# Kernel optimization log

Hardware: AMD Instinct MI355X
Metric: run time of the kernel (lower is better)

The kernel has to match this reference:

```python
import jax, jax.numpy as jnp
import numpy as np

N_HEAD = 16

def _rope_cos_sin(T, head_dim, dtype):
    # inv_freq over even indices, freqs [T, head_dim//2]
    inv_freq = 1.0 / (10000.0 ** (jnp.arange(0, head_dim, 2, dtype=jnp.float32) / head_dim))
    t = jnp.arange(T, dtype=jnp.float32)
    freqs = t[:, None] * inv_freq[None, :]
    cos = jnp.cos(freqs).astype(dtype)[None, :, None, :]  # [1,T,1,hd/2]
    sin = jnp.sin(freqs).astype(dtype)[None, :, None, :]
    return cos, sin

def _apply_rope(x, cos, sin):
    # x: [B,T,H,hd]; interleaved halves as in the torch module
    x1, x2 = x[..., ::2], x[..., 1::2]
    return jnp.concatenate([x1 * cos - x2 * sin, x1 * sin + x2 * cos], axis=-1)

def setup_inputs() -> dict:
    key = jax.random.key(0)
    k1, k2, k3 = jax.random.split(key, 3)
    B, T, C = 2, 2048, 1024
    x = jax.random.normal(k1, (B, T, C), dtype=jnp.float32)
    # causal mask (mask==0 positions get -inf), broadcast over B and heads
    attn_mask = jnp.tril(jnp.ones((T, T), dtype=bool))[None, None, :, :]
    w_qkv = jax.random.normal(k2, (C, 3 * C), dtype=jnp.float32) * (1.0 / np.sqrt(C))
    w_out = jax.random.normal(k3, (C, C), dtype=jnp.float32) * (1.0 / np.sqrt(C))
    return {"x": x, "attn_mask": attn_mask, "w_qkv": w_qkv, "w_out": w_out}

def reference(x, attn_mask, w_qkv, w_out):
    B, T, C = x.shape
    H = N_HEAD
    hd = C // H
    qkv = x @ w_qkv  # [B,T,3C]
    q, k, v = jnp.split(qkv, 3, axis=2)
    q = q.reshape(B, T, H, hd)
    k = k.reshape(B, T, H, hd)
    v = v.reshape(B, T, H, hd)
    cos, sin = _rope_cos_sin(T, hd, x.dtype)
    q = _apply_rope(q, cos, sin)
    k = _apply_rope(k, cos, sin)
    scale = 1.0 / np.sqrt(hd).astype(np.float32)
    att = jnp.einsum('bthd,bshd->bhts', q, k) * scale  # [B,H,T,T]
    att = jnp.where(attn_mask, att, -jnp.inf)
    att = jax.nn.softmax(att, axis=-1)
    out = jnp.einsum('bhts,bshd->bthd', att, v).reshape(B, T, C)
    out = out @ w_out
    k_t = jnp.transpose(k, (0, 2, 1, 3))  # [B,H,T,hd]
    v_t = jnp.transpose(v, (0, 2, 1, 3))
    return out, k_t, v_t
```

## Files before the change

kernel.cpp:

```cpp
#include <hip/hip_runtime.h>

#define T_SEQ 2048
#define NH    16
#define HD    64
#define CDIM  1024
#define BDIM  2

using floatx4 = __attribute__((ext_vector_type(4))) float;
using bf16x8  = __attribute__((ext_vector_type(8))) __bf16;
using half4   = __attribute__((ext_vector_type(4))) _Float16;
typedef unsigned short u16;

__device__ __forceinline__ u16 f2bf(float f) {
  unsigned int u = __float_as_uint(f);
  u += 0x7fffu + ((u >> 16) & 1u);
  return (u16)(u >> 16);
}
__device__ __forceinline__ float bf2f(u16 h) {
  return __uint_as_float(((unsigned int)h) << 16);
}
__device__ __forceinline__ u16 f2h(float f) {
  union { _Float16 h; u16 u; } c; c.h = (_Float16)f; return c.u;
}
__device__ __forceinline__ unsigned pk2h(float a, float b) {
  return __builtin_bit_cast(unsigned, __builtin_amdgcn_cvt_pkrtz(a, b));
}
__device__ __forceinline__ void gld16(const void* g, const void* l) {
  __builtin_amdgcn_global_load_lds(
      (const __attribute__((address_space(1))) unsigned int*)(unsigned long long)g,
      (__attribute__((address_space(3))) unsigned int*)(unsigned int)(unsigned long long)l,
      16, 0, 0);
}

__global__ __launch_bounds__(256) void cast_bf16(const float* __restrict__ in,
                                                 u16* __restrict__ out, int n4) {
  int i = blockIdx.x * 256 + threadIdx.x;
  if (i < n4) {
    float4 v = ((const float4*)in)[i];
    ushort4 o;
    o.x = f2bf(v.x); o.y = f2bf(v.y); o.z = f2bf(v.z); o.w = f2bf(v.w);
    ((ushort4*)out)[i] = o;
  }
}

__global__ __launch_bounds__(256) void transpose_cast(const float* __restrict__ W,
                                                      u16* __restrict__ WT,
                                                      int K, int N) {
  __shared__ float tile[32][33];
  int n0 = blockIdx.x * 32, k0 = blockIdx.y * 32;
  int tx = threadIdx.x, ty = threadIdx.y;
#pragma unroll
  for (int i = 0; i < 32; i += 8)
    tile[ty + i][tx] = W[(size_t)(k0 + ty + i) * N + n0 + tx];
  __syncthreads();
#pragma unroll
  for (int i = 0; i < 32; i += 8)
    WT[(size_t)(n0 + ty + i) * K + k0 + tx] = f2bf(tile[tx][ty + i]);
}

template <bool OUT_F32>
__global__ __launch_bounds__(256) void gemm_bt(const u16* __restrict__ A,
                                               const u16* __restrict__ BT,
                                               float* __restrict__ Cf,
                                               u16* __restrict__ Cb,
                                               int M, int N, int K) {
  __shared__ u16 As[128 * 32];
  __shared__ u16 Bs[128 * 32];
  const int tid  = threadIdx.x;
  const int lane = tid & 63, wave = tid >> 6;
  const int quad = lane >> 4, l16 = lane & 15;
  const int wm = (wave & 1) * 64, wn = (wave >> 1) * 64;
  const int row0 = blockIdx.x * 128, col0 = blockIdx.y * 128;
  const int srow = tid >> 2;
  const int sc   = tid & 3;
  const int sgc  = (sc ^ ((srow >> 1) & 3)) * 8;
  floatx4 acc[4][4] = {};
  for (int k0 = 0; k0 < K; k0 += 32) {
    __syncthreads();
    gld16(A  + (size_t)(row0 + srow     ) * K + k0 + sgc, &As[srow * 32 + sc * 8]);
    gld16(A  + (size_t)(row0 + srow + 64) * K + k0 + sgc, &As[(srow + 64) * 32 + sc * 8]);
    gld16(BT + (size_t)(col0 + srow     ) * K + k0 + sgc, &Bs[srow * 32 + sc * 8]);
    gld16(BT + (size_t)(col0 + srow + 64) * K + k0 + sgc, &Bs[(srow + 64) * 32 + sc * 8]);
    __syncthreads();
    bf16x8 af[4], bfv[4];
#pragma unroll
    for (int mt = 0; mt < 4; mt++) {
      int r = wm + mt * 16 + l16;
      af[mt] = *(const bf16x8*)&As[r * 32 + (quad ^ ((r >> 1) & 3)) * 8];
    }
#pragma unroll
    for (int nt = 0; nt < 4; nt++) {
      int r = wn + nt * 16 + l16;
      bfv[nt] = *(const bf16x8*)&Bs[r * 32 + (quad ^ ((r >> 1) & 3)) * 8];
    }
#pragma unroll
    for (int mt = 0; mt < 4; mt++)
#pragma unroll
      for (int nt = 0; nt < 4; nt++)
        acc[mt][nt] = __builtin_amdgcn_mfma_f32_16x16x32_bf16(af[mt], bfv[nt], acc[mt][nt], 0, 0, 0);
  }
#pragma unroll
  for (int mt = 0; mt < 4; mt++)
#pragma unroll
    for (int nt = 0; nt < 4; nt++)
#pragma unroll
      for (int r = 0; r < 4; r++) {
        int row = row0 + wm + mt * 16 + quad * 4 + r;
        int col = col0 + wn + nt * 16 + l16;
        float v = acc[mt][nt][r];
        if (OUT_F32) Cf[(size_t)row * N + col] = v;
        else         Cb[(size_t)row * N + col] = f2bf(v);
      }
}

__global__ __launch_bounds__(256) void rope_qk(const u16* __restrict__ qkv,
                                               u16* __restrict__ qf16,
                                               u16* __restrict__ kf16,
                                               float* __restrict__ kt_out) {
  int gid = blockIdx.x * 4 + (threadIdx.x >> 6);
  int d   = threadIdx.x & 63;
  int t   = gid & (T_SEQ - 1);
  int h   = (gid >> 11) & 15;
  int b   = gid >> 15;
  const u16* qrow = qkv + ((size_t)(b * T_SEQ + t)) * 3072 + h * 64;
  int i = d & 31;
  unsigned int qp = *(const unsigned int*)(qrow + 2 * i);
  unsigned int kp = *(const unsigned int*)(qrow + 1024 + 2 * i);
  float q1 = bf2f((u16)qp), q2 = bf2f((u16)(qp >> 16));
  float k1 = bf2f((u16)kp), k2 = bf2f((u16)(kp >> 16));
  float inv = expf((float)i * -0.28782313662425572f);
  float ang = (float)t * inv;
  float sn = sinf(ang), cs = cosf(ang);
  float qv = (d < 32) ? (q1 * cs - q2 * sn) : (q1 * sn + q2 * cs);
  float kv = (d < 32) ? (k1 * cs - k2 * sn) : (k1 * sn + k2 * cs);
  size_t o = (size_t)gid * 64 + d;
  qf16[o] = f2h(qv * 0.18033688011112042f);
  kf16[o] = f2h(kv);
  kt_out[o] = kv;
}

__global__ __launch_bounds__(256) void v_pack(const u16* __restrict__ qkv,
                                              float* __restrict__ vt_out,
                                              u16* __restrict__ vtf) {
  __shared__ float tile[64][65];
  int blk = blockIdx.x;
  int t0 = (blk & 31) * 64;
  int bh = blk >> 5;
  int b = bh >> 4, h = bh & 15;
  int tx = threadIdx.x & 63, ty = threadIdx.x >> 6;
#pragma unroll
  for (int i = ty; i < 64; i += 4) {
    float v = bf2f(qkv[((size_t)(b * T_SEQ + t0 + i)) * 3072 + 2048 + h * 64 + tx]);
    tile[i][tx] = v;
    vt_out[((size_t)bh * T_SEQ + t0 + i) * 64 + tx] = v;
  }
  __syncthreads();
#pragma unroll
  for (int i = ty; i < 64; i += 4)
    vtf[((size_t)bh * 64 + i) * T_SEQ + t0 + tx] = f2h(tile[tx][i]);
}

__global__ __launch_bounds__(256) void attn_fused(const u16* __restrict__ qf16,
                                                  const u16* __restrict__ kf16,
                                                  const u16* __restrict__ vtf,
                                                  u16* __restrict__ Ob) {
  __shared__ u16 Ks[128 * 64];
  __shared__ u16 Vts[64 * 128];
  const int tid = threadIdx.x;
  const int lane = tid & 63, wave = tid >> 6;
  const int quad = lane >> 4, l16 = lane & 15;
  const int qh2 = quad >> 1, ql2 = (quad & 1) * 4;
  const int qt2 = 31 - (blockIdx.x >> 5);
  const int bh  = blockIdx.x & 31;
  const int t0  = qt2 * 64;
  const int tw  = t0 + wave * 16;

  const u16* Qg = qf16 + ((size_t)bh * T_SEQ + tw) * HD;
  half4 qfrag[4];
#pragma unroll
  for (int kc = 0; kc < 4; kc++)
    qfrag[kc] = *(const half4*)&Qg[(size_t)l16 * HD + kc * 16 + quad * 4];

  floatx4 oacc[4] = {};
  float mrow = -1e30f, lrow = 0.f;
  const int nkt = (qt2 >> 1) + 1;

  for (int kt = 0; kt < nkt; kt++) {
    __syncthreads();
    const size_t koff = ((size_t)bh * T_SEQ + kt * 128) * HD;
    const u16* Vg = vtf + (size_t)bh * HD * T_SEQ + kt * 128;
#pragma unroll
    for (int j = 0; j < 4; j++) {
      int t2 = j * 256 + tid;
      int r = t2 >> 3, c = t2 & 7;
      gld16(kf16 + koff + r * HD + (c ^ (r & 7)) * 8, &Ks[t2 * 8]);
    }
#pragma unroll
    for (int j = 0; j < 4; j++) {
      int t2 = j * 256 + tid;
      int r = t2 >> 4, c = t2 & 15;
      gld16(Vg + (size_t)r * T_SEQ + (c ^ (r & 15)) * 8, &Vts[t2 * 8]);
    }
    __syncthreads();

    floatx4 sacc[8] = {};
#pragma unroll
    for (int kc = 0; kc < 4; kc++)
#pragma unroll
      for (int st = 0; st < 8; st++) {
        int srow = st * 16 + l16;
        half4 ak = *(const half4*)&Ks[srow * 64 + (((kc * 2 + qh2) ^ (srow & 7)) * 8) + ql2];
        sacc[st] = __builtin_amdgcn_mfma_f32_16x16x16f16(ak, qfrag[kc], sacc[st], 0, 0, 0);
      }
    if (kt == nkt - 1) {
      int tg = tw + l16;
#pragma unroll
      for (int st = 0; st < 8; st++) {
        int sg = kt * 128 + st * 16 + quad * 4;
#pragma unroll
        for (int r = 0; r < 4; r++)
          if (sg + r > tg) sacc[st][r] = -1e30f;
      }
    }
    {
      floatx4 vm = sacc[0];
#pragma unroll
      for (int st = 1; st < 8; st++) {
        vm[0] = fmaxf(vm[0], sacc[st][0]); vm[1] = fmaxf(vm[1], sacc[st][1]);
        vm[2] = fmaxf(vm[2], sacc[st][2]); vm[3] = fmaxf(vm[3], sacc[st][3]);
      }
      float mx = fmaxf(fmaxf(vm[0], vm[1]), fmaxf(vm[2], vm[3]));
      mx = fmaxf(mx, __shfl_xor(mx, 16));
      mx = fmaxf(mx, __shfl_xor(mx, 32));
      float mnew = fmaxf(mrow, mx);
      float alpha = exp2f(mrow - mnew);
      mrow = mnew;
      floatx4 vs = {0.f, 0.f, 0.f, 0.f};
#pragma unroll
      for (int st = 0; st < 8; st++) {
#pragma unroll
        for (int r = 0; r < 4; r++) sacc[st][r] = exp2f(sacc[st][r] - mnew);
        vs += sacc[st];
      }
      float rs = (vs[0] + vs[1]) + (vs[2] + vs[3]);
      rs += __shfl_xor(rs, 16);
      rs += __shfl_xor(rs, 32);
      lrow = lrow * alpha + rs;
#pragma unroll
      for (int dt = 0; dt < 4; dt++) oacc[dt] *= alpha;
    }
#pragma unroll
    for (int st = 0; st < 8; st++) {
      union { unsigned u[2]; half4 h; } pc;
      pc.u[0] = pk2h(sacc[st][0], sacc[st][1]);
      pc.u[1] = pk2h(sacc[st][2], sacc[st][3]);
      half4 bp = pc.h;
#pragma unroll
      for (int dt = 0; dt < 4; dt++) {
        int drow = dt * 16 + l16;
        half4 av = *(const half4*)&Vts[drow * 128 + (((st * 2 + qh2) ^ (drow & 15)) * 8) + ql2];
        oacc[dt] = __builtin_amdgcn_mfma_f32_16x16x16f16(av, bp, oacc[dt], 0, 0, 0);
      }
    }
  }
  const int b = bh >> 4, h = bh & 15;
  {
    int t = tw + l16;
    float invl = 1.f / lrow;
#pragma unroll
    for (int dt = 0; dt < 4; dt++) {
      int d0 = dt * 16 + quad * 4;
      ushort4 o;
      o.x = f2bf(oacc[dt][0] * invl);
      o.y = f2bf(oacc[dt][1] * invl);
      o.z = f2bf(oacc[dt][2] * invl);
      o.w = f2bf(oacc[dt][3] * invl);
      *(ushort4*)&Ob[((size_t)(b * T_SEQ) + t) * CDIM + h * HD + d0] = o;
    }
  }
}

extern "C" void kernel_launch(void* const* d_in, const int* in_sizes, int n_in,
                              void* d_out, int out_size, void* d_ws, size_t ws_size,
                              hipStream_t stream) {
  const float* x     = (const float*)d_in[0];
  const float* w_qkv = (const float*)d_in[2];
  const float* w_out = (const float*)d_in[3];
  float* out    = (float*)d_out;
  float* kt_out = out + (size_t)BDIM * T_SEQ * CDIM;
  float* vt_out = kt_out + (size_t)BDIM * T_SEQ * CDIM;

  const size_t F = (size_t)4194304;
  char* base = (char*)d_ws;
  u16* xb   = (u16*)base;
  u16* wqT  = xb + F;
  u16* woT  = wqT + (size_t)3145728;
  u16* qkvb = woT + (size_t)1048576;
  u16* qf16 = qkvb + (size_t)3 * F;
  u16* kf16 = qf16 + F;
  u16* vtf  = (u16*)base;
  u16* Ob   = kf16 + F;

  cast_bf16<<<4096, 256, 0, stream>>>(x, xb, 1048576);
  transpose_cast<<<dim3(96, 32), dim3(32, 8), 0, stream>>>(w_qkv, wqT, 1024, 3072);
  transpose_cast<<<dim3(32, 32), dim3(32, 8), 0, stream>>>(w_out, woT, 1024, 1024);
  gemm_bt<false><<<dim3(32, 24), 256, 0, stream>>>(xb, wqT, (float*)nullptr, qkvb, 4096, 3072, 1024);
  rope_qk<<<16384, 256, 0, stream>>>(qkvb, qf16, kf16, kt_out);
  v_pack<<<1024, 256, 0, stream>>>(qkvb, vt_out, vtf);
  attn_fused<<<1024, 256, 0, stream>>>(qf16, kf16, vtf, Ob);
  gemm_bt<true><<<dim3(32, 8), 256, 0, stream>>>(Ob, woT, out, (u16*)nullptr, 4096, 1024, 1024);
}
```

Baseline: 234.2 us.

## Merge preprocessing kernels, pair causal tiles per attention block, use 32-wide MFMA

Three preprocessing launches (x cast and two weight transposes) become one kernel, and rope and V packing become one kernel, cutting launch overhead. The attention kernel now handles two query tiles per block (j and 31-j), so each block does the same amount of causal work, and it launches 512 blocks instead of 1024. The QK^T product moves from 16x16x16 f16 MFMA to 16x16x32 f16 with half8 fragments, which halves the instruction count for that step. The cost is fewer attention blocks in flight, which gives less parallelism to hide latency.

After: 224.7 us. -4.1%, faster.

```diff
diff --git a/kernel.cpp b/kernel.cpp
--- a/kernel.cpp
+++ b/kernel.cpp
@@ -9,6 +9,7 @@
 using floatx4 = __attribute__((ext_vector_type(4))) float;
 using bf16x8  = __attribute__((ext_vector_type(8))) __bf16;
 using half4   = __attribute__((ext_vector_type(4))) _Float16;
+using half8   = __attribute__((ext_vector_type(8))) _Float16;
 typedef unsigned short u16;
 
 __device__ __forceinline__ u16 f2bf(float f) {
@@ -32,23 +33,32 @@
       16, 0, 0);
 }
 
-__global__ __launch_bounds__(256) void cast_bf16(const float* __restrict__ in,
-                                                 u16* __restrict__ out, int n4) {
-  int i = blockIdx.x * 256 + threadIdx.x;
-  if (i < n4) {
-    float4 v = ((const float4*)in)[i];
+__global__ __launch_bounds__(256) void preproc(const float* __restrict__ x,
+                                               const float* __restrict__ w_qkv,
+                                               const float* __restrict__ w_out,
+                                               u16* __restrict__ xb,
+                                               u16* __restrict__ wqT,
+                                               u16* __restrict__ woT) {
+  __shared__ float tile[32][33];
+  int blk = blockIdx.x, tid = threadIdx.x;
+  if (blk < 4096) {
+    int i = blk * 256 + tid;
+    float4 v = ((const float4*)x)[i];
     ushort4 o;
     o.x = f2bf(v.x); o.y = f2bf(v.y); o.z = f2bf(v.z); o.w = f2bf(v.w);
-    ((ushort4*)out)[i] = o;
-  }
-}
-
-__global__ __launch_bounds__(256) void transpose_cast(const float* __restrict__ W,
-                                                      u16* __restrict__ WT,
-                                                      int K, int N) {
-  __shared__ float tile[32][33];
-  int n0 = blockIdx.x * 32, k0 = blockIdx.y * 32;
-  int tx = threadIdx.x, ty = threadIdx.y;
+    ((ushort4*)xb)[i] = o;
+    return;
+  }
+  const float* W; u16* WT; int K, N, bx, by;
+  if (blk < 4096 + 3072) {
+    int idx = blk - 4096; W = w_qkv; WT = wqT; K = 1024; N = 3072;
+    bx = idx % 96; by = idx / 96;
+  } else {
+    int idx = blk - 7168; W = w_out; WT = woT; K = 1024; N = 1024;
+    bx = idx & 31; by = idx >> 5;
+  }
+  int n0 = bx * 32, k0 = by * 32;
+  int tx = tid & 31, ty = tid >> 5;
 #pragma unroll
   for (int i = 0; i < 32; i += 8)
     tile[ty + i][tx] = W[(size_t)(k0 + ty + i) * N + n0 + tx];
@@ -113,39 +123,40 @@
       }
 }
 
-__global__ __launch_bounds__(256) void rope_qk(const u16* __restrict__ qkv,
-                                               u16* __restrict__ qf16,
-                                               u16* __restrict__ kf16,
-                                               float* __restrict__ kt_out) {
-  int gid = blockIdx.x * 4 + (threadIdx.x >> 6);
-  int d   = threadIdx.x & 63;
-  int t   = gid & (T_SEQ - 1);
-  int h   = (gid >> 11) & 15;
-  int b   = gid >> 15;
-  const u16* qrow = qkv + ((size_t)(b * T_SEQ + t)) * 3072 + h * 64;
-  int i = d & 31;
-  unsigned int qp = *(const unsigned int*)(qrow + 2 * i);
-  unsigned int kp = *(const unsigned int*)(qrow + 1024 + 2 * i);
-  float q1 = bf2f((u16)qp), q2 = bf2f((u16)(qp >> 16));
-  float k1 = bf2f((u16)kp), k2 = bf2f((u16)(kp >> 16));
-  float inv = expf((float)i * -0.28782313662425572f);
-  float ang = (float)t * inv;
-  float sn = sinf(ang), cs = cosf(ang);
-  float qv = (d < 32) ? (q1 * cs - q2 * sn) : (q1 * sn + q2 * cs);
-  float kv = (d < 32) ? (k1 * cs - k2 * sn) : (k1 * sn + k2 * cs);
-  size_t o = (size_t)gid * 64 + d;
-  qf16[o] = f2h(qv * 0.18033688011112042f);
-  kf16[o] = f2h(kv);
-  kt_out[o] = kv;
-}
-
-__global__ __launch_bounds__(256) void v_pack(const u16* __restrict__ qkv,
-                                              float* __restrict__ vt_out,
-                                              u16* __restrict__ vtf) {
+__global__ __launch_bounds__(256) void rope_vpack(const u16* __restrict__ qkv,
+                                                  u16* __restrict__ qf16,
+                                                  u16* __restrict__ kf16,
+                                                  float* __restrict__ kt_out,
+                                                  float* __restrict__ vt_out,
+                                                  u16* __restrict__ vtf) {
+  int blk = blockIdx.x;
+  if (blk < 16384) {
+    int gid = blk * 4 + (threadIdx.x >> 6);
+    int d   = threadIdx.x & 63;
+    int t   = gid & (T_SEQ - 1);
+    int h   = (gid >> 11) & 15;
+    int b   = gid >> 15;
+    const u16* qrow = qkv + ((size_t)(b * T_SEQ + t)) * 3072 + h * 64;
+    int i = d & 31;
+    unsigned int qp = *(const unsigned int*)(qrow + 2 * i);
+    unsigned int kp = *(const unsigned int*)(qrow + 1024 + 2 * i);
+    float q1 = bf2f((u16)qp), q2 = bf2f((u16)(qp >> 16));
+    float k1 = bf2f((u16)kp), k2 = bf2f((u16)(kp >> 16));
+    float inv = expf((float)i * -0.28782313662425572f);
+    float ang = (float)t * inv;
+    float sn = sinf(ang), cs = cosf(ang);
+    float qv = (d < 32) ? (q1 * cs - q2 * sn) : (q1 * sn + q2 * cs);
+    float kv = (d < 32) ? (k1 * cs - k2 * sn) : (k1 * sn + k2 * cs);
+    size_t o = (size_t)gid * 64 + d;
+    qf16[o] = f2h(qv * 0.18033688011112042f);
+    kf16[o] = f2h(kv);
+    kt_out[o] = kv;
+    return;
+  }
   __shared__ float tile[64][65];
-  int blk = blockIdx.x;
-  int t0 = (blk & 31) * 64;
-  int bh = blk >> 5;
+  int b2 = blk - 16384;
+  int t0 = (b2 & 31) * 64;
+  int bh = b2 >> 5;
   int b = bh >> 4, h = bh & 15;
   int tx = threadIdx.x & 63, ty = threadIdx.x >> 6;
 #pragma unroll
@@ -170,112 +181,115 @@
   const int lane = tid & 63, wave = tid >> 6;
   const int quad = lane >> 4, l16 = lane & 15;
   const int qh2 = quad >> 1, ql2 = (quad & 1) * 4;
-  const int qt2 = 31 - (blockIdx.x >> 5);
+  const int j   = blockIdx.x >> 5;
   const int bh  = blockIdx.x & 31;
-  const int t0  = qt2 * 64;
-  const int tw  = t0 + wave * 16;
-
-  const u16* Qg = qf16 + ((size_t)bh * T_SEQ + tw) * HD;
-  half4 qfrag[4];
-#pragma unroll
-  for (int kc = 0; kc < 4; kc++)
-    qfrag[kc] = *(const half4*)&Qg[(size_t)l16 * HD + kc * 16 + quad * 4];
-
-  floatx4 oacc[4] = {};
-  float mrow = -1e30f, lrow = 0.f;
-  const int nkt = (qt2 >> 1) + 1;
-
-  for (int kt = 0; kt < nkt; kt++) {
-    __syncthreads();
-    const size_t koff = ((size_t)bh * T_SEQ + kt * 128) * HD;
-    const u16* Vg = vtf + (size_t)bh * HD * T_SEQ + kt * 128;
-#pragma unroll
-    for (int j = 0; j < 4; j++) {
-      int t2 = j * 256 + tid;
-      int r = t2 >> 3, c = t2 & 7;
-      gld16(kf16 + koff + r * HD + (c ^ (r & 7)) * 8, &Ks[t2 * 8]);
-    }
-#pragma unroll
-    for (int j = 0; j < 4; j++) {
-      int t2 = j * 256 + tid;
-      int r = t2 >> 4, c = t2 & 15;
-      gld16(Vg + (size_t)r * T_SEQ + (c ^ (r & 15)) * 8, &Vts[t2 * 8]);
-    }
-    __syncthreads();
-
-    floatx4 sacc[8] = {};
-#pragma unroll
-    for (int kc = 0; kc < 4; kc++)
+  const int b = bh >> 4, h = bh & 15;
+
+#pragma unroll 1
+  for (int s2 = 0; s2 < 2; s2++) {
+    const int qt2 = s2 ? j : (31 - j);
+    const int tw  = qt2 * 64 + wave * 16;
+    const u16* Qg = qf16 + ((size_t)bh * T_SEQ + tw) * HD;
+    half8 qfrag[2];
+#pragma unroll
+    for (int kc = 0; kc < 2; kc++)
+      qfrag[kc] = *(const half8*)&Qg[(size_t)l16 * HD + kc * 32 + quad * 8];
+
+    floatx4 oacc[4] = {};
+    float mrow = -1e30f, lrow = 0.f;
+    const int nkt = (qt2 >> 1) + 1;
+
+    for (int kt = 0; kt < nkt; kt++) {
+      __syncthreads();
+      const size_t koff = ((size_t)bh * T_SEQ + kt * 128) * HD;
+      const u16* Vg = vtf + (size_t)bh * HD * T_SEQ + kt * 128;
+#pragma unroll
+      for (int jj = 0; jj < 4; jj++) {
+        int t2 = jj * 256 + tid;
+        int r = t2 >> 3, c = t2 & 7;
+        gld16(kf16 + koff + r * HD + (c ^ (r & 7)) * 8, &Ks[t2 * 8]);
+      }
+#pragma unroll
+      for (int jj = 0; jj < 4; jj++) {
+        int t2 = jj * 256 + tid;
+        int r = t2 >> 4, c = t2 & 15;
+        gld16(Vg + (size_t)r * T_SEQ + (c ^ (r & 15)) * 8, &Vts[t2 * 8]);
+      }
+      __syncthreads();
+
+      floatx4 sacc[8] = {};
+#pragma unroll
+      for (int kc = 0; kc < 2; kc++)
+#pragma unroll
+        for (int st = 0; st < 8; st++) {
+          int srow = st * 16 + l16;
+          half8 ak = *(const half8*)&Ks[srow * 64 + (((kc * 4 + quad) ^ (srow & 7)) * 8)];
+          sacc[st] = __builtin_amdgcn_mfma_f32_16x16x32_f16(ak, qfrag[kc], sacc[st], 0, 0, 0);
+        }
+      if (kt == nkt - 1) {
+        int tg = tw + l16;
+#pragma unroll
+        for (int st = 0; st < 8; st++) {
+          int sg = kt * 128 + st * 16 + quad * 4;
+#pragma unroll
+          for (int r = 0; r < 4; r++)
+            if (sg + r > tg) sacc[st][r] = -1e30f;
+        }
+      }
+      {
+        floatx4 vm = sacc[0];
+#pragma unroll
+        for (int st = 1; st < 8; st++) {
+          vm[0] = fmaxf(vm[0], sacc[st][0]); vm[1] = fmaxf(vm[1], sacc[st][1]);
+          vm[2] = fmaxf(vm[2], sacc[st][2]); vm[3] = fmaxf(vm[3], sacc[st][3]);
+        }
+        float mx = fmaxf(fmaxf(vm[0], vm[1]), fmaxf(vm[2], vm[3]));
+        mx = fmaxf(mx, __shfl_xor(mx, 16));
+        mx = fmaxf(mx, __shfl_xor(mx, 32));
+        float mnew = fmaxf(mrow, mx);
+        float alpha = exp2f(mrow - mnew);
+        mrow = mnew;
+        floatx4 vs = {0.f, 0.f, 0.f, 0.f};
+#pragma unroll
+        for (int st = 0; st < 8; st++) {
+#pragma unroll
+          for (int r = 0; r < 4; r++) sacc[st][r] = exp2f(sacc[st][r] - mnew);
+          vs += sacc[st];
+        }
+        float rs = (vs[0] + vs[1]) + (vs[2] + vs[3]);
+        rs += __shfl_xor(rs, 16);
+        rs += __shfl_xor(rs, 32);
+        lrow = lrow * alpha + rs;
+#pragma unroll
+        for (int dt = 0; dt < 4; dt++) oacc[dt] *= alpha;
+      }
 #pragma unroll
       for (int st = 0; st < 8; st++) {
-        int srow = st * 16 + l16;
-        half4 ak = *(const half4*)&Ks[srow * 64 + (((kc * 2 + qh2) ^ (srow & 7)) * 8) + ql2];
-        sacc[st] = __builtin_amdgcn_mfma_f32_16x16x16f16(ak, qfrag[kc], sacc[st], 0, 0, 0);
-      }
-    if (kt == nkt - 1) {
-      int tg = tw + l16;
-#pragma unroll
-      for (int st = 0; st < 8; st++) {
-        int sg = kt * 128 + st * 16 + quad * 4;
-#pragma unroll
-        for (int r = 0; r < 4; r++)
-          if (sg + r > tg) sacc[st][r] = -1e30f;
+        union { unsigned u[2]; half4 h; } pc;
+        pc.u[0] = pk2h(sacc[st][0], sacc[st][1]);
+        pc.u[1] = pk2h(sacc[st][2], sacc[st][3]);
+        half4 bp = pc.h;
+#pragma unroll
+        for (int dt = 0; dt < 4; dt++) {
+          int drow = dt * 16 + l16;
+          half4 av = *(const half4*)&Vts[drow * 128 + (((st * 2 + qh2) ^ (drow & 15)) * 8) + ql2];
+          oacc[dt] = __builtin_amdgcn_mfma_f32_16x16x16f16(av, bp, oacc[dt], 0, 0, 0);
+        }
       }
     }
     {
-      floatx4 vm = sacc[0];
-#pragma unroll
-      for (int st = 1; st < 8; st++) {
-        vm[0] = fmaxf(vm[0], sacc[st][0]); vm[1] = fmaxf(vm[1], sacc[st][1]);
-        vm[2] = fmaxf(vm[2], sacc[st][2]); vm[3] = fmaxf(vm[3], sacc[st][3]);
-      }
-      float mx = fmaxf(fmaxf(vm[0], vm[1]), fmaxf(vm[2], vm[3]));
-      mx = fmaxf(mx, __shfl_xor(mx, 16));
-      mx = fmaxf(mx, __shfl_xor(mx, 32));
-      float mnew = fmaxf(mrow, mx);
-      float alpha = exp2f(mrow - mnew);
-      mrow = mnew;
-      floatx4 vs = {0.f, 0.f, 0.f, 0.f};
-#pragma unroll
-      for (int st = 0; st < 8; st++) {
-#pragma unroll
-        for (int r = 0; r < 4; r++) sacc[st][r] = exp2f(sacc[st][r] - mnew);
-        vs += sacc[st];
-      }
-      float rs = (vs[0] + vs[1]) + (vs[2] + vs[3]);
-      rs += __shfl_xor(rs, 16);
-      rs += __shfl_xor(rs, 32);
-      lrow = lrow * alpha + rs;
-#pragma unroll
-      for (int dt = 0; dt < 4; dt++) oacc[dt] *= alpha;
-    }
-#pragma unroll
-    for (int st = 0; st < 8; st++) {
-      union { unsigned u[2]; half4 h; } pc;
-      pc.u[0] = pk2h(sacc[st][0], sacc[st][1]);
-      pc.u[1] = pk2h(sacc[st][2], sacc[st][3]);
-      half4 bp = pc.h;
+      int t = tw + l16;
+      float invl = 1.f / lrow;
 #pragma unroll
       for (int dt = 0; dt < 4; dt++) {
-        int drow = dt * 16 + l16;
-        half4 av = *(const half4*)&Vts[drow * 128 + (((st * 2 + qh2) ^ (drow & 15)) * 8) + ql2];
-        oacc[dt] = __builtin_amdgcn_mfma_f32_16x16x16f16(av, bp, oacc[dt], 0, 0, 0);
-      }
-    }
-  }
-  const int b = bh >> 4, h = bh & 15;
-  {
-    int t = tw + l16;
-    float invl = 1.f / lrow;
-#pragma unroll
-    for (int dt = 0; dt < 4; dt++) {
-      int d0 = dt * 16 + quad * 4;
-      ushort4 o;
-      o.x = f2bf(oacc[dt][0] * invl);
-      o.y = f2bf(oacc[dt][1] * invl);
-      o.z = f2bf(oacc[dt][2] * invl);
-      o.w = f2bf(oacc[dt][3] * invl);
-      *(ushort4*)&Ob[((size_t)(b * T_SEQ) + t) * CDIM + h * HD + d0] = o;
+        int d0 = dt * 16 + quad * 4;
+        ushort4 o;
+        o.x = f2bf(oacc[dt][0] * invl);
+        o.y = f2bf(oacc[dt][1] * invl);
+        o.z = f2bf(oacc[dt][2] * invl);
+        o.w = f2bf(oacc[dt][3] * invl);
+        *(ushort4*)&Ob[((size_t)(b * T_SEQ) + t) * CDIM + h * HD + d0] = o;
+      }
     }
   }
 }
@@ -301,12 +315,9 @@
   u16* vtf  = (u16*)base;
   u16* Ob   = kf16 + F;
 
-  cast_bf16<<<4096, 256, 0, stream>>>(x, xb, 1048576);
-  transpose_cast<<<dim3(96, 32), dim3(32, 8), 0, stream>>>(w_qkv, wqT, 1024, 3072);
-  transpose_cast<<<dim3(32, 32), dim3(32, 8), 0, stream>>>(w_out, woT, 1024, 1024);
+  preproc<<<8192, 256, 0, stream>>>(x, w_qkv, w_out, xb, wqT, woT);
   gemm_bt<false><<<dim3(32, 24), 256, 0, stream>>>(xb, wqT, (float*)nullptr, qkvb, 4096, 3072, 1024);
-  rope_qk<<<16384, 256, 0, stream>>>(qkvb, qf16, kf16, kt_out);
-  v_pack<<<1024, 256, 0, stream>>>(qkvb, vt_out, vtf);
-  attn_fused<<<1024, 256, 0, stream>>>(qf16, kf16, vtf, Ob);
+  rope_vpack<<<17408, 256, 0, stream>>>(qkvb, qf16, kf16, kt_out, vt_out, vtf);
+  attn_fused<<<512, 256, 0, stream>>>(qf16, kf16, vtf, Ob);
   gemm_bt<true><<<dim3(32, 8), 256, 0, stream>>>(Ob, woT, out, (u16*)nullptr, 4096, 1024, 1024);
 }
```
